# Kernel optimization log

Hardware: AMD Instinct MI355X
Metric: run time of the kernel (lower is better)

Reference implementation:

```python
import jax, jax.numpy as jnp
import numpy as np

B, L, C, V, SU, SI, D = 256, 3, 8, 20, 32, 32, 64
NE, NR = 200000, 32


def _xavier(key, shape):
    fan_in, fan_out = shape[-2], shape[-1]
    a = (6.0 / (fan_in + fan_out)) ** 0.5
    return jax.random.uniform(key, shape, jnp.float32, -a, a)


def setup_inputs() -> dict:
    key = jax.random.key(0)
    ks = jax.random.split(key, 18)

    def triple(k, S):
        k1, k2 = jax.random.split(k)
        ents = jax.random.randint(k1, (B, L, C, 2, S), 0, NE, dtype=jnp.int32)
        rels = jax.random.randint(k2, (B, L, C, 1, S), 0, NR, dtype=jnp.int32)
        # rows: [head, relation, tail]
        return jnp.concatenate([ents[:, :, :, :1], rels, ents[:, :, :, 1:]], axis=3)

    entity_emb = _xavier(ks[0], (NE + 1, D)).at[NE].set(0.0)  # padding row zeroed
    relation_emb = _xavier(ks[1], (NR, D))
    return {
        "user_course_videos": jax.random.randint(ks[2], (B, C, V), 0, NE, dtype=jnp.int32),
        "items": jax.random.randint(ks[3], (B,), 0, NE, dtype=jnp.int32),
        "neg_items": jax.random.randint(ks[4], (B,), 0, NE, dtype=jnp.int32),
        "user_triple_set": triple(ks[5], SU),
        "item_triple_set": triple(ks[6], SI),
        "neg_item_triple_set": triple(ks[7], SI),
        "user_course_list": jax.random.randint(ks[8], (B, C), 0, NE, dtype=jnp.int32),
        "item_course_list": jax.random.randint(ks[9], (B, C), 0, NE, dtype=jnp.int32),
        "neg_item_course_list": jax.random.randint(ks[10], (B, C), 0, NE, dtype=jnp.int32),
        "entity_emb": entity_emb,
        "relation_emb": relation_emb,
        "W": _xavier(ks[11], (2 * D, D)),
        "W_ht": _xavier(ks[12], (2 * D, D)),
        "W_course": _xavier(ks[13], (D, D)),
        "W_video": _xavier(ks[14], (D, D)),
    }


def _normalize(x):
    n = jnp.linalg.norm(x, axis=-1, keepdims=True)
    return x / jnp.maximum(n, 1e-12)


def _layer_emb(E, R, W, W_ht, ts, cce, vce):
    # ts: [B, L, C, 3, S]; cce/vce: [B, D]
    h = E[ts[:, :, :, 0, :]]  # [B,L,C,S,D]
    r = R[ts[:, :, :, 1, :]]
    t = E[ts[:, :, :, 2, :]]
    hr_W = jnp.concatenate([h, r], axis=-1) @ W  # [B,L,C,S,D]
    p = jax.nn.softmax(jax.nn.sigmoid(jnp.einsum('blcsd,bd->blcs', hr_W, cce)), axis=-1)[..., None]
    o = p * t
    if vce is not None:
        ht_W = jnp.concatenate([h, t], axis=-1) @ W_ht
        p2 = jax.nn.sigmoid(jnp.einsum('blcsd,bd->blcs', ht_W, vce))[..., None]
        o = p2 * o
    return o.sum(axis=-2)  # [B,L,C,D]


def _run_user(E, R, W, W_ht, W_course, W_video, ucv, uts, ucl):
    vc = E[ucv].sum(axis=-2)                                     # [B,C,D]
    cce = (E[ucl] + jax.nn.sigmoid(vc @ W_course)).mean(axis=-2)  # [B,D]
    vce = jax.nn.sigmoid(vc.mean(axis=-2) @ W_video)              # [B,D]
    u = _layer_emb(E, R, W, W_ht, uts, cce, vce)                  # [B,L,C,D]
    u = _normalize(jnp.transpose(u, (0, 2, 1, 3)))                # [B,C,L,D]; dropout is identity (eval)
    return u.sum(axis=2).mean(axis=1)                             # [B,D]


def _run_item(E, R, W, W_ht, items, its, icl):
    ie = E[items]                                                 # [B,D]
    cce = ie + ie * E[icl[:, 1:]].mean(axis=-2)                   # [B,D]
    c = _layer_emb(E, R, W, W_ht, its, cce, None)                 # [B,L,C,D]
    c = _normalize(jnp.transpose(c, (0, 2, 1, 3))).sum(axis=2)    # [B,C,D]
    cw = jax.nn.sigmoid(jnp.einsum('bcd,bd->bc', c[:, 1:], c[:, 0]))[..., None]  # [B,C-1,1]
    p_cw = jax.nn.softmax(cw, axis=1)
    mean_cf = (p_cw * c[:, 1:]).sum(axis=1)                       # [B,D]
    alpha = jax.nn.sigmoid((ie * mean_cf).sum(axis=-1, keepdims=True))
    return alpha / (1.0 + alpha) * mean_cf + c[:, 0] + ie


def reference(user_course_videos, items, neg_items, user_triple_set, item_triple_set,
              neg_item_triple_set, user_course_list, item_course_list, neg_item_course_list,
              entity_emb, relation_emb, W, W_ht, W_course, W_video):
    u = _run_user(entity_emb, relation_emb, W, W_ht, W_course, W_video,
                  user_course_videos, user_triple_set, user_course_list)
    c = _run_item(entity_emb, relation_emb, W, W_ht, items, item_triple_set, item_course_list)
    n_c = _run_item(entity_emb, relation_emb, W, W_ht, neg_items, neg_item_triple_set, neg_item_course_list)
    scores = (u * c).sum(axis=1)
    neg_scores = (u * n_c).sum(axis=1)
    return scores, neg_scores
```

## Files before the change

kernel.cpp:

```cpp
#include <hip/hip_runtime.h>
#include <math.h>

#define BB 256
#define LL 3
#define CC 8
#define VV 20
#define SS 32
#define DD 64
#define NG (BB * LL * CC)

typedef float v4f __attribute__((ext_vector_type(4)));

__device__ __forceinline__ float sigmoidf_(float x) { return 1.0f / (1.0f + __expf(-x)); }
__device__ __forceinline__ float dot4v_(v4f a, v4f b) {
    return a[0] * b[0] + a[1] * b[1] + a[2] * b[2] + a[3] * b[3];
}
__device__ __forceinline__ void gload4(v4f& dst, const float* p) {
    asm volatile("global_load_dwordx4 %0, %1, off" : "=v"(dst) : "v"(p));
}

__global__ __launch_bounds__(256) void prologue(
    const float* __restrict__ E, const int* __restrict__ ucv, const int* __restrict__ ucl,
    const int* __restrict__ items, const int* __restrict__ icl, const int* __restrict__ negs,
    const int* __restrict__ ncl, const float* __restrict__ W, const float* __restrict__ W_ht,
    const float* __restrict__ Wc, const float* __restrict__ Wv, float* __restrict__ wcce_u,
    float* __restrict__ whv_u, float* __restrict__ wcce_i, float* __restrict__ wcce_n,
    float* __restrict__ ie_i, float* __restrict__ ie_n) {
    int b = blockIdx.x, tid = threadIdx.x;
    int d = tid & 63, q = tid >> 6;
    __shared__ float vcs[CC][DD];
    __shared__ float part[4][DD];
    __shared__ float part2[4][DD];
    __shared__ float cce_u_s[DD], vce_u_s[DD], cce_i_s[DD], cce_n_s[DD], vmean_s[DD];
    __shared__ float ie_s[2][DD];

    float p1 = 0.f;
    for (int cc = 0; cc < 2; ++cc) {
        int c = q + cc * 4;
        const int* iv = ucv + (b * CC + c) * VV;
        float a = 0.f;
#pragma unroll
        for (int v = 0; v < VV; ++v) a += E[(long)iv[v] * DD + d];
        vcs[c][d] = a;
        p1 += E[(long)ucl[b * CC + c] * DD + d];
    }
    part[q][d] = p1;
    __syncthreads();
    {
        float sacc = 0.f;
        for (int cc = 0; cc < 2; ++cc) {
            int c = q + cc * 4;
            float m = 0.f;
#pragma unroll 8
            for (int k = 0; k < DD; ++k) m += vcs[c][k] * Wc[k * DD + d];
            sacc += sigmoidf_(m);
        }
        part2[q][d] = sacc;
    }
    __syncthreads();
    if (q == 0) {
        float s = 0.f;
#pragma unroll
        for (int i = 0; i < 4; ++i) s += part[i][d] + part2[i][d];
        cce_u_s[d] = s * (1.f / CC);
        float vm = 0.f;
#pragma unroll
        for (int c = 0; c < CC; ++c) vm += vcs[c][d];
        vmean_s[d] = vm * (1.f / CC);
    }
    __syncthreads();
    {
        float m = 0.f;
        for (int k = q * 16; k < q * 16 + 16; ++k) m += vmean_s[k] * Wv[k * DD + d];
        part[q][d] = m;
    }
    {
        const int* cl = (q < 2) ? icl : ncl;
        int c0 = (q & 1) ? 5 : 1, c1 = (q & 1) ? 8 : 5;
        float m = 0.f;
        for (int c = c0; c < c1; ++c) m += E[(long)cl[b * CC + c] * DD + d];
        part2[q][d] = m;
        if (q == 1) ie_s[0][d] = E[(long)items[b] * DD + d];
        if (q == 3) ie_s[1][d] = E[(long)negs[b] * DD + d];
    }
    __syncthreads();
    if (q == 0) {
        vce_u_s[d] = sigmoidf_(part[0][d] + part[1][d] + part[2][d] + part[3][d]);
        float ie = ie_s[0][d];
        cce_i_s[d] = ie * (1.f + (part2[0][d] + part2[1][d]) * (1.f / 7.f));
        ie_i[b * DD + d] = ie;
    } else if (q == 1) {
        float ie = ie_s[1][d];
        cce_n_s[d] = ie * (1.f + (part2[2][d] + part2[3][d]) * (1.f / 7.f));
        ie_n[b * DD + d] = ie;
    }
    __syncthreads();
    {
        int k = tid & 127, sel = tid >> 7;
        const float* wr = (sel ? W_ht : W) + k * DD;
        const float* wr2 = W + k * DD;
        const float* v1 = sel ? vce_u_s : cce_u_s;
        const float* v2 = sel ? cce_n_s : cce_i_s;
        float a = 0.f, c2 = 0.f;
#pragma unroll 8
        for (int kk = 0; kk < DD; ++kk) {
            a += wr[kk] * v1[kk];
            c2 += wr2[kk] * v2[kk];
        }
        if (sel == 0) {
            wcce_u[b * 128 + k] = a;
            wcce_i[b * 128 + k] = c2;
        } else {
            whv_u[b * 128 + k] = a;
            wcce_n[b * 128 + k] = c2;
        }
    }
}

__global__ __launch_bounds__(256, 3) void layer_all(
    const float* __restrict__ E, const float* __restrict__ R, const int* __restrict__ uts,
    const int* __restrict__ its, const int* __restrict__ nts, const float* __restrict__ wcce_u,
    const float* __restrict__ whv_u, const float* __restrict__ wcce_i,
    const float* __restrict__ wcce_n, float* __restrict__ o_all) {
    int tid = threadIdx.x;
    int w = tid >> 6, lane = tid & 63;
    int f = lane & 15, grp = lane >> 4;
    int gg = blockIdx.x * 4 + w;
    int seg = gg / NG;
    int g = gg - seg * NG;
    int b = g / (LL * CC);
    const int* ts = (seg == 0) ? uts : (seg == 1) ? its : nts;
    const float* wcp = (seg == 0) ? wcce_u : (seg == 1) ? wcce_i : wcce_n;
    const bool has_p2 = (seg == 0);
    const int* tg = ts + (long)g * 3 * SS;

    int idx_a = tg[lane];
    int idx_b = tg[64 + (lane & 31)];

    int hix[8], rix[8], tix[8];
#pragma unroll
    for (int p = 0; p < 8; ++p) {
        int row = p * 4 + grp;
        hix[p] = __shfl(idx_a, row, 64);
        rix[p] = __shfl(idx_a, 32 + row, 64);
        tix[p] = __shfl(idx_b, row, 64);
    }

    v4f wc_h, wc_r, wh_h, wh_t;
    gload4(wc_h, wcp + b * 128 + f * 4);
    gload4(wc_r, wcp + b * 128 + 64 + f * 4);
    if (has_p2) {
        gload4(wh_h, whv_u + b * 128 + f * 4);
        gload4(wh_t, whv_u + b * 128 + 64 + f * 4);
    }
    v4f hv[8], rv[8], t4[8];
#pragma unroll
    for (int p = 0; p < 8; ++p) gload4(hv[p], E + (long)hix[p] * DD + f * 4);
#pragma unroll
    for (int p = 0; p < 8; ++p) gload4(rv[p], R + (long)rix[p] * DD + f * 4);
#pragma unroll
    for (int p = 0; p < 8; ++p) gload4(t4[p], E + (long)tix[p] * DD + f * 4);

    asm volatile("s_waitcnt vmcnt(8)");
    __builtin_amdgcn_sched_barrier(0);

    float s1[8];
#pragma unroll
    for (int p = 0; p < 8; ++p) {
        float a1 = dot4v_(hv[p], wc_h) + dot4v_(rv[p], wc_r);
#pragma unroll
        for (int m = 1; m < 16; m <<= 1) a1 += __shfl_xor(a1, m, 64);
        s1[p] = a1;
    }
    float mx = -1e30f;
#pragma unroll
    for (int p = 0; p < 8; ++p) {
        s1[p] = sigmoidf_(s1[p]);
        mx = fmaxf(mx, s1[p]);
    }
    mx = fmaxf(mx, __shfl_xor(mx, 16, 64));
    mx = fmaxf(mx, __shfl_xor(mx, 32, 64));
    float se = 0.f;
#pragma unroll
    for (int p = 0; p < 8; ++p) {
        s1[p] = __expf(s1[p] - mx);
        se += s1[p];
    }
    se += __shfl_xor(se, 16, 64);
    se += __shfl_xor(se, 32, 64);
    float inv = 1.f / se;

    __builtin_amdgcn_sched_barrier(0);
    asm volatile("s_waitcnt vmcnt(0)");
    __builtin_amdgcn_sched_barrier(0);

    float s2[8];
    if (has_p2) {
#pragma unroll
        for (int p = 0; p < 8; ++p) {
            float a2 = dot4v_(hv[p], wh_h) + dot4v_(t4[p], wh_t);
#pragma unroll
            for (int m = 1; m < 16; m <<= 1) a2 += __shfl_xor(a2, m, 64);
            s2[p] = a2;
        }
    }
    float4 oacc = make_float4(0.f, 0.f, 0.f, 0.f);
#pragma unroll
    for (int p = 0; p < 8; ++p) {
        float wgt = s1[p] * inv;
        if (has_p2) wgt *= sigmoidf_(s2[p]);
        oacc.x += wgt * t4[p][0];
        oacc.y += wgt * t4[p][1];
        oacc.z += wgt * t4[p][2];
        oacc.w += wgt * t4[p][3];
    }
#pragma unroll
    for (int m = 16; m <= 32; m <<= 1) {
        oacc.x += __shfl_xor(oacc.x, m, 64);
        oacc.y += __shfl_xor(oacc.y, m, 64);
        oacc.z += __shfl_xor(oacc.z, m, 64);
        oacc.w += __shfl_xor(oacc.w, m, 64);
    }
    float qq = oacc.x * oacc.x + oacc.y * oacc.y + oacc.z * oacc.z + oacc.w * oacc.w;
#pragma unroll
    for (int m = 1; m < 16; m <<= 1) qq += __shfl_xor(qq, m, 64);
    float innorm = 1.f / fmaxf(sqrtf(qq), 1e-12f);
    if (grp == 0) {
        oacc.x *= innorm;
        oacc.y *= innorm;
        oacc.z *= innorm;
        oacc.w *= innorm;
        *(float4*)(o_all + (long)gg * DD + f * 4) = oacc;
    }
}

__global__ __launch_bounds__(192) void postlude(const float* __restrict__ o_all,
                                                const float* __restrict__ ie_i,
                                                const float* __restrict__ ie_n,
                                                float* __restrict__ out) {
    int b = blockIdx.x, tid = threadIdx.x;
    int w = tid / 64, d = tid & 63;
    __shared__ float u_s[DD], ci_s[DD], cn_s[DD];
    if (w == 0) {
        const float* o_u = o_all + (long)b * LL * CC * DD;
        float acc = 0.f;
#pragma unroll
        for (int lc = 0; lc < LL * CC; ++lc) acc += o_u[lc * DD + d];
        u_s[d] = acc * (1.f / CC);
    } else {
        const float* o_c = o_all + ((long)w * NG + (long)b * LL * CC) * DD;
        const float* ie_buf = (w == 1) ? ie_i : ie_n;
        float cs[CC];
#pragma unroll
        for (int c = 0; c < CC; ++c) {
            float a = 0.f;
#pragma unroll
            for (int l = 0; l < LL; ++l) a += o_c[(l * CC + c) * DD + d];
            cs[c] = a;
        }
        float p[CC - 1];
        float mx = -1e30f;
        for (int c = 0; c < CC - 1; ++c) {
            float dd2 = cs[0] * cs[c + 1];
#pragma unroll
            for (int m = 32; m > 0; m >>= 1) dd2 += __shfl_xor(dd2, m, 64);
            p[c] = sigmoidf_(dd2);
            mx = fmaxf(mx, p[c]);
        }
        float se = 0.f;
        for (int c = 0; c < CC - 1; ++c) {
            p[c] = __expf(p[c] - mx);
            se += p[c];
        }
        float mcf = 0.f;
        for (int c = 0; c < CC - 1; ++c) mcf += (p[c] / se) * cs[c + 1];
        float ie = ie_buf[b * DD + d];
        float ad = ie * mcf;
#pragma unroll
        for (int m = 32; m > 0; m >>= 1) ad += __shfl_xor(ad, m, 64);
        float alpha = sigmoidf_(ad);
        float res = alpha / (1.f + alpha) * mcf + cs[0] + ie;
        if (w == 1)
            ci_s[d] = res;
        else
            cn_s[d] = res;
    }
    __syncthreads();
    if (w == 0) {
        float uv = u_s[d];
        float s1 = uv * ci_s[d];
        float s2 = uv * cn_s[d];
#pragma unroll
        for (int m = 32; m > 0; m >>= 1) {
            s1 += __shfl_xor(s1, m, 64);
            s2 += __shfl_xor(s2, m, 64);
        }
        if (d == 0) {
            out[b] = s1;
            out[BB + b] = s2;
        }
    }
}

extern "C" void kernel_launch(void* const* d_in, const int* in_sizes, int n_in,
                              void* d_out, int out_size, void* d_ws, size_t ws_size,
                              hipStream_t stream) {
    const int* ucv = (const int*)d_in[0];
    const int* items = (const int*)d_in[1];
    const int* negs = (const int*)d_in[2];
    const int* uts = (const int*)d_in[3];
    const int* its = (const int*)d_in[4];
    const int* nts = (const int*)d_in[5];
    const int* ucl = (const int*)d_in[6];
    const int* icl = (const int*)d_in[7];
    const int* ncl = (const int*)d_in[8];
    const float* E = (const float*)d_in[9];
    const float* R = (const float*)d_in[10];
    const float* W = (const float*)d_in[11];
    const float* W_ht = (const float*)d_in[12];
    const float* Wc = (const float*)d_in[13];
    const float* Wv = (const float*)d_in[14];

    float* ws = (float*)d_ws;
    float* wcce_u = ws;
    float* whv_u = wcce_u + BB * 128;
    float* wcce_i = whv_u + BB * 128;
    float* wcce_n = wcce_i + BB * 128;
    float* ie_i = wcce_n + BB * 128;
    float* ie_n = ie_i + BB * DD;
    float* o_all = ie_n + BB * DD;

    prologue<<<BB, 256, 0, stream>>>(E, ucv, ucl, items, icl, negs, ncl, W, W_ht, Wc, Wv,
                                     wcce_u, whv_u, wcce_i, wcce_n, ie_i, ie_n);
    layer_all<<<(3 * NG) / 4, 256, 0, stream>>>(E, R, uts, its, nts, wcce_u, whv_u, wcce_i,
                                                wcce_n, o_all);
    postlude<<<BB, 192, 0, stream>>>(o_all, ie_i, ie_n, (float*)d_out);
}
```

Baseline: 65.15 us.

## Gather triple embeddings directly into LDS via global_load_lds with one-wave blocks

Replaces the register-destined gathers of head, relation and tail embeddings with global_load_lds transfers into a 24KB shared staging buffer, then reads the rows back from LDS. Each block now holds a single wave and handles one group, so the launch has four times as many blocks. The goal is to cut VGPR pressure from the 24 in-flight vector loads and raise occupancy for this latency-bound gather. In exchange it adds an LDS round trip and a large per-block LDS footprint that caps waves per CU. It also relies on the vmcnt-based waits covering the LDS-bound DMA loads.

```diff
diff --git a/kernel.cpp b/kernel.cpp
--- a/kernel.cpp
+++ b/kernel.cpp
@@ -15,8 +15,10 @@
 __device__ __forceinline__ float dot4v_(v4f a, v4f b) {
     return a[0] * b[0] + a[1] * b[1] + a[2] * b[2] + a[3] * b[3];
 }
-__device__ __forceinline__ void gload4(v4f& dst, const float* p) {
-    asm volatile("global_load_dwordx4 %0, %1, off" : "=v"(dst) : "v"(p));
+__device__ __forceinline__ void gl_lds16(const float* gsrc, float* lptr) {
+    __builtin_amdgcn_global_load_lds(
+        (const __attribute__((address_space(1))) void*)(uintptr_t)gsrc,
+        (__attribute__((address_space(3))) void*)(uint32_t)(uintptr_t)lptr, 16, 0, 0);
 }
 
 __global__ __launch_bounds__(256) void prologue(
@@ -117,15 +119,14 @@
     }
 }
 
-__global__ __launch_bounds__(256, 3) void layer_all(
+__global__ __launch_bounds__(64) void layer_all(
     const float* __restrict__ E, const float* __restrict__ R, const int* __restrict__ uts,
     const int* __restrict__ its, const int* __restrict__ nts, const float* __restrict__ wcce_u,
     const float* __restrict__ whv_u, const float* __restrict__ wcce_i,
     const float* __restrict__ wcce_n, float* __restrict__ o_all) {
-    int tid = threadIdx.x;
-    int w = tid >> 6, lane = tid & 63;
+    int lane = threadIdx.x;
     int f = lane & 15, grp = lane >> 4;
-    int gg = blockIdx.x * 4 + w;
+    int gg = blockIdx.x;
     int seg = gg / NG;
     int g = gg - seg * NG;
     int b = g / (LL * CC);
@@ -134,40 +135,46 @@
     const bool has_p2 = (seg == 0);
     const int* tg = ts + (long)g * 3 * SS;
 
+    __shared__ float stage[96 * DD];
+
     int idx_a = tg[lane];
     int idx_b = tg[64 + (lane & 31)];
 
-    int hix[8], rix[8], tix[8];
+    v4f wch = *(const v4f*)(wcp + b * 128 + f * 4);
+    v4f wcr = *(const v4f*)(wcp + b * 128 + 64 + f * 4);
+    v4f whh = {0.f, 0.f, 0.f, 0.f}, wht = {0.f, 0.f, 0.f, 0.f};
+    if (has_p2) {
+        whh = *(const v4f*)(whv_u + b * 128 + f * 4);
+        wht = *(const v4f*)(whv_u + b * 128 + 64 + f * 4);
+    }
+    __builtin_amdgcn_sched_barrier(0);
+
+#pragma unroll
+    for (int q = 0; q < 8; ++q) {
+        int hi = __shfl(idx_a, q * 4 + grp, 64);
+        gl_lds16(E + (long)hi * DD + f * 4, stage + (q * 4) * DD);
+    }
+#pragma unroll
+    for (int q = 0; q < 8; ++q) {
+        int ri = __shfl(idx_a, 32 + q * 4 + grp, 64);
+        gl_lds16(R + (long)ri * DD + f * 4, stage + (32 + q * 4) * DD);
+    }
+#pragma unroll
+    for (int q = 0; q < 8; ++q) {
+        int ti = __shfl(idx_b, q * 4 + grp, 64);
+        gl_lds16(E + (long)ti * DD + f * 4, stage + (64 + q * 4) * DD);
+    }
+
+    asm volatile("s_waitcnt vmcnt(8)" ::: "memory");
+    __builtin_amdgcn_sched_barrier(0);
+
+    v4f hv[8];
+    float s1[8];
 #pragma unroll
     for (int p = 0; p < 8; ++p) {
-        int row = p * 4 + grp;
-        hix[p] = __shfl(idx_a, row, 64);
-        rix[p] = __shfl(idx_a, 32 + row, 64);
-        tix[p] = __shfl(idx_b, row, 64);
-    }
-
-    v4f wc_h, wc_r, wh_h, wh_t;
-    gload4(wc_h, wcp + b * 128 + f * 4);
-    gload4(wc_r, wcp + b * 128 + 64 + f * 4);
-    if (has_p2) {
-        gload4(wh_h, whv_u + b * 128 + f * 4);
-        gload4(wh_t, whv_u + b * 128 + 64 + f * 4);
-    }
-    v4f hv[8], rv[8], t4[8];
-#pragma unroll
-    for (int p = 0; p < 8; ++p) gload4(hv[p], E + (long)hix[p] * DD + f * 4);
-#pragma unroll
-    for (int p = 0; p < 8; ++p) gload4(rv[p], R + (long)rix[p] * DD + f * 4);
-#pragma unroll
-    for (int p = 0; p < 8; ++p) gload4(t4[p], E + (long)tix[p] * DD + f * 4);
-
-    asm volatile("s_waitcnt vmcnt(8)");
-    __builtin_amdgcn_sched_barrier(0);
-
-    float s1[8];
-#pragma unroll
-    for (int p = 0; p < 8; ++p) {
-        float a1 = dot4v_(hv[p], wc_h) + dot4v_(rv[p], wc_r);
+        hv[p] = *(const v4f*)(stage + (p * 4 + grp) * DD + f * 4);
+        v4f rv = *(const v4f*)(stage + (32 + p * 4 + grp) * DD + f * 4);
+        float a1 = dot4v_(hv[p], wch) + dot4v_(rv, wcr);
 #pragma unroll
         for (int m = 1; m < 16; m <<= 1) a1 += __shfl_xor(a1, m, 64);
         s1[p] = a1;
@@ -191,28 +198,24 @@
     float inv = 1.f / se;
 
     __builtin_amdgcn_sched_barrier(0);
-    asm volatile("s_waitcnt vmcnt(0)");
+    asm volatile("s_waitcnt vmcnt(0)" ::: "memory");
     __builtin_amdgcn_sched_barrier(0);
 
-    float s2[8];
-    if (has_p2) {
-#pragma unroll
-        for (int p = 0; p < 8; ++p) {
-            float a2 = dot4v_(hv[p], wh_h) + dot4v_(t4[p], wh_t);
+    float4 oacc = make_float4(0.f, 0.f, 0.f, 0.f);
+#pragma unroll
+    for (int p = 0; p < 8; ++p) {
+        v4f t4 = *(const v4f*)(stage + (64 + p * 4 + grp) * DD + f * 4);
+        float wgt = s1[p] * inv;
+        if (has_p2) {
+            float a2 = dot4v_(hv[p], whh) + dot4v_(t4, wht);
 #pragma unroll
             for (int m = 1; m < 16; m <<= 1) a2 += __shfl_xor(a2, m, 64);
-            s2[p] = a2;
-        }
-    }
-    float4 oacc = make_float4(0.f, 0.f, 0.f, 0.f);
-#pragma unroll
-    for (int p = 0; p < 8; ++p) {
-        float wgt = s1[p] * inv;
-        if (has_p2) wgt *= sigmoidf_(s2[p]);
-        oacc.x += wgt * t4[p][0];
-        oacc.y += wgt * t4[p][1];
-        oacc.z += wgt * t4[p][2];
-        oacc.w += wgt * t4[p][3];
+            wgt *= sigmoidf_(a2);
+        }
+        oacc.x += wgt * t4[0];
+        oacc.y += wgt * t4[1];
+        oacc.z += wgt * t4[2];
+        oacc.w += wgt * t4[3];
     }
 #pragma unroll
     for (int m = 16; m <= 32; m <<= 1) {
@@ -332,7 +335,7 @@
 
     prologue<<<BB, 256, 0, stream>>>(E, ucv, ucl, items, icl, negs, ncl, W, W_ht, Wc, Wv,
                                      wcce_u, whv_u, wcce_i, wcce_n, ie_i, ie_n);
-    layer_all<<<(3 * NG) / 4, 256, 0, stream>>>(E, R, uts, its, nts, wcce_u, whv_u, wcce_i,
-                                                wcce_n, o_all);
+    layer_all<<<3 * NG, 64, 0, stream>>>(E, R, uts, its, nts, wcce_u, whv_u, wcce_i,
+                                         wcce_n, o_all);
     postlude<<<BB, 192, 0, stream>>>(o_all, ie_i, ie_n, (float*)d_out);
 }
```

New measurement: 82.61 us. 1.27x slower.

## Make layer kernel persistent grid-stride and drop inline-asm loads and waitcnts

Applied to the files above, without the earlier changes.

The layer kernel goes from one wave per group with 4-wave blocks to a persistent grid-stride loop over 4096 waves in 2-wave blocks with a higher occupancy hint. The hand-written global_load asm and explicit vmcnt waits are replaced by plain vector loads, so the compiler now schedules loads and the s2 computation. The aim is to cut block launch overhead and let the compiler overlap loads across loop iterations. In exchange it gives up the manual split that started the softmax while the tail loads were still in flight, and each wave now handles several groups in sequence.

```diff
diff --git a/kernel.cpp b/kernel.cpp
--- a/kernel.cpp
+++ b/kernel.cpp
@@ -8,15 +8,13 @@
 #define SS 32
 #define DD 64
 #define NG (BB * LL * CC)
+#define NWAVES 4096
 
 typedef float v4f __attribute__((ext_vector_type(4)));
 
 __device__ __forceinline__ float sigmoidf_(float x) { return 1.0f / (1.0f + __expf(-x)); }
 __device__ __forceinline__ float dot4v_(v4f a, v4f b) {
     return a[0] * b[0] + a[1] * b[1] + a[2] * b[2] + a[3] * b[3];
-}
-__device__ __forceinline__ void gload4(v4f& dst, const float* p) {
-    asm volatile("global_load_dwordx4 %0, %1, off" : "=v"(dst) : "v"(p));
 }
 
 __global__ __launch_bounds__(256) void prologue(
@@ -117,120 +115,113 @@
     }
 }
 
-__global__ __launch_bounds__(256, 3) void layer_all(
+__global__ __launch_bounds__(128, 8) void layer_all(
     const float* __restrict__ E, const float* __restrict__ R, const int* __restrict__ uts,
     const int* __restrict__ its, const int* __restrict__ nts, const float* __restrict__ wcce_u,
     const float* __restrict__ whv_u, const float* __restrict__ wcce_i,
     const float* __restrict__ wcce_n, float* __restrict__ o_all) {
     int tid = threadIdx.x;
-    int w = tid >> 6, lane = tid & 63;
+    int lane = tid & 63;
     int f = lane & 15, grp = lane >> 4;
-    int gg = blockIdx.x * 4 + w;
-    int seg = gg / NG;
-    int g = gg - seg * NG;
-    int b = g / (LL * CC);
-    const int* ts = (seg == 0) ? uts : (seg == 1) ? its : nts;
-    const float* wcp = (seg == 0) ? wcce_u : (seg == 1) ? wcce_i : wcce_n;
-    const bool has_p2 = (seg == 0);
-    const int* tg = ts + (long)g * 3 * SS;
-
-    int idx_a = tg[lane];
-    int idx_b = tg[64 + (lane & 31)];
-
-    int hix[8], rix[8], tix[8];
-#pragma unroll
-    for (int p = 0; p < 8; ++p) {
-        int row = p * 4 + grp;
-        hix[p] = __shfl(idx_a, row, 64);
-        rix[p] = __shfl(idx_a, 32 + row, 64);
-        tix[p] = __shfl(idx_b, row, 64);
-    }
-
-    v4f wc_h, wc_r, wh_h, wh_t;
-    gload4(wc_h, wcp + b * 128 + f * 4);
-    gload4(wc_r, wcp + b * 128 + 64 + f * 4);
-    if (has_p2) {
-        gload4(wh_h, whv_u + b * 128 + f * 4);
-        gload4(wh_t, whv_u + b * 128 + 64 + f * 4);
-    }
-    v4f hv[8], rv[8], t4[8];
-#pragma unroll
-    for (int p = 0; p < 8; ++p) gload4(hv[p], E + (long)hix[p] * DD + f * 4);
-#pragma unroll
-    for (int p = 0; p < 8; ++p) gload4(rv[p], R + (long)rix[p] * DD + f * 4);
-#pragma unroll
-    for (int p = 0; p < 8; ++p) gload4(t4[p], E + (long)tix[p] * DD + f * 4);
-
-    asm volatile("s_waitcnt vmcnt(8)");
-    __builtin_amdgcn_sched_barrier(0);
-
-    float s1[8];
-#pragma unroll
-    for (int p = 0; p < 8; ++p) {
-        float a1 = dot4v_(hv[p], wc_h) + dot4v_(rv[p], wc_r);
-#pragma unroll
-        for (int m = 1; m < 16; m <<= 1) a1 += __shfl_xor(a1, m, 64);
-        s1[p] = a1;
-    }
-    float mx = -1e30f;
-#pragma unroll
-    for (int p = 0; p < 8; ++p) {
-        s1[p] = sigmoidf_(s1[p]);
-        mx = fmaxf(mx, s1[p]);
-    }
-    mx = fmaxf(mx, __shfl_xor(mx, 16, 64));
-    mx = fmaxf(mx, __shfl_xor(mx, 32, 64));
-    float se = 0.f;
-#pragma unroll
-    for (int p = 0; p < 8; ++p) {
-        s1[p] = __expf(s1[p] - mx);
-        se += s1[p];
-    }
-    se += __shfl_xor(se, 16, 64);
-    se += __shfl_xor(se, 32, 64);
-    float inv = 1.f / se;
-
-    __builtin_amdgcn_sched_barrier(0);
-    asm volatile("s_waitcnt vmcnt(0)");
-    __builtin_amdgcn_sched_barrier(0);
-
-    float s2[8];
-    if (has_p2) {
-#pragma unroll
-        for (int p = 0; p < 8; ++p) {
-            float a2 = dot4v_(hv[p], wh_h) + dot4v_(t4[p], wh_t);
-#pragma unroll
-            for (int m = 1; m < 16; m <<= 1) a2 += __shfl_xor(a2, m, 64);
-            s2[p] = a2;
-        }
-    }
-    float4 oacc = make_float4(0.f, 0.f, 0.f, 0.f);
-#pragma unroll
-    for (int p = 0; p < 8; ++p) {
-        float wgt = s1[p] * inv;
-        if (has_p2) wgt *= sigmoidf_(s2[p]);
-        oacc.x += wgt * t4[p][0];
-        oacc.y += wgt * t4[p][1];
-        oacc.z += wgt * t4[p][2];
-        oacc.w += wgt * t4[p][3];
-    }
-#pragma unroll
-    for (int m = 16; m <= 32; m <<= 1) {
-        oacc.x += __shfl_xor(oacc.x, m, 64);
-        oacc.y += __shfl_xor(oacc.y, m, 64);
-        oacc.z += __shfl_xor(oacc.z, m, 64);
-        oacc.w += __shfl_xor(oacc.w, m, 64);
-    }
-    float qq = oacc.x * oacc.x + oacc.y * oacc.y + oacc.z * oacc.z + oacc.w * oacc.w;
-#pragma unroll
-    for (int m = 1; m < 16; m <<= 1) qq += __shfl_xor(qq, m, 64);
-    float innorm = 1.f / fmaxf(sqrtf(qq), 1e-12f);
-    if (grp == 0) {
-        oacc.x *= innorm;
-        oacc.y *= innorm;
-        oacc.z *= innorm;
-        oacc.w *= innorm;
-        *(float4*)(o_all + (long)gg * DD + f * 4) = oacc;
+    int wave0 = blockIdx.x * 2 + (tid >> 6);
+
+    for (int gg = wave0; gg < 3 * NG; gg += NWAVES) {
+        int seg = gg / NG;
+        int g = gg - seg * NG;
+        int b = g / (LL * CC);
+        const int* ts = (seg == 0) ? uts : (seg == 1) ? its : nts;
+        const float* wcp = (seg == 0) ? wcce_u : (seg == 1) ? wcce_i : wcce_n;
+        const bool has_p2 = (seg == 0);
+        const int* tg = ts + (long)g * 3 * SS;
+
+        int idx_a = tg[lane];
+        int idx_b = tg[64 + (lane & 31)];
+        int hix[8], rix[8], tix[8];
+#pragma unroll
+        for (int p = 0; p < 8; ++p) {
+            int row = p * 4 + grp;
+            hix[p] = __shfl(idx_a, row, 64);
+            rix[p] = __shfl(idx_a, 32 + row, 64);
+            tix[p] = __shfl(idx_b, row, 64);
+        }
+        const v4f* wc4 = (const v4f*)(wcp + b * 128);
+        v4f wc_h = wc4[f], wc_r = wc4[f + 16];
+        v4f wh_h = {0.f, 0.f, 0.f, 0.f}, wh_t = wh_h;
+        if (has_p2) {
+            const v4f* wh4 = (const v4f*)(whv_u + b * 128);
+            wh_h = wh4[f];
+            wh_t = wh4[f + 16];
+        }
+        v4f hv[8], rv[8], t4[8];
+#pragma unroll
+        for (int p = 0; p < 8; ++p) hv[p] = *(const v4f*)(E + (long)hix[p] * DD + f * 4);
+#pragma unroll
+        for (int p = 0; p < 8; ++p) rv[p] = *(const v4f*)(R + (long)rix[p] * DD + f * 4);
+#pragma unroll
+        for (int p = 0; p < 8; ++p) t4[p] = *(const v4f*)(E + (long)tix[p] * DD + f * 4);
+
+        float s1[8], s2[8];
+#pragma unroll
+        for (int p = 0; p < 8; ++p) {
+            float a1 = dot4v_(hv[p], wc_h) + dot4v_(rv[p], wc_r);
+#pragma unroll
+            for (int m = 1; m < 16; m <<= 1) a1 += __shfl_xor(a1, m, 64);
+            s1[p] = a1;
+        }
+        if (has_p2) {
+#pragma unroll
+            for (int p = 0; p < 8; ++p) {
+                float a2 = dot4v_(hv[p], wh_h) + dot4v_(t4[p], wh_t);
+#pragma unroll
+                for (int m = 1; m < 16; m <<= 1) a2 += __shfl_xor(a2, m, 64);
+                s2[p] = a2;
+            }
+        }
+        float mx = -1e30f;
+#pragma unroll
+        for (int p = 0; p < 8; ++p) {
+            s1[p] = sigmoidf_(s1[p]);
+            mx = fmaxf(mx, s1[p]);
+        }
+        mx = fmaxf(mx, __shfl_xor(mx, 16, 64));
+        mx = fmaxf(mx, __shfl_xor(mx, 32, 64));
+        float se = 0.f;
+#pragma unroll
+        for (int p = 0; p < 8; ++p) {
+            s1[p] = __expf(s1[p] - mx);
+            se += s1[p];
+        }
+        se += __shfl_xor(se, 16, 64);
+        se += __shfl_xor(se, 32, 64);
+        float inv = 1.f / se;
+        float4 oacc = make_float4(0.f, 0.f, 0.f, 0.f);
+#pragma unroll
+        for (int p = 0; p < 8; ++p) {
+            float wgt = s1[p] * inv;
+            if (has_p2) wgt *= sigmoidf_(s2[p]);
+            oacc.x += wgt * t4[p][0];
+            oacc.y += wgt * t4[p][1];
+            oacc.z += wgt * t4[p][2];
+            oacc.w += wgt * t4[p][3];
+        }
+#pragma unroll
+        for (int m = 16; m <= 32; m <<= 1) {
+            oacc.x += __shfl_xor(oacc.x, m, 64);
+            oacc.y += __shfl_xor(oacc.y, m, 64);
+            oacc.z += __shfl_xor(oacc.z, m, 64);
+            oacc.w += __shfl_xor(oacc.w, m, 64);
+        }
+        float qq = oacc.x * oacc.x + oacc.y * oacc.y + oacc.z * oacc.z + oacc.w * oacc.w;
+#pragma unroll
+        for (int m = 1; m < 16; m <<= 1) qq += __shfl_xor(qq, m, 64);
+        float innorm = 1.f / fmaxf(sqrtf(qq), 1e-12f);
+        if (grp == 0) {
+            oacc.x *= innorm;
+            oacc.y *= innorm;
+            oacc.z *= innorm;
+            oacc.w *= innorm;
+            *(float4*)(o_all + (long)gg * DD + f * 4) = oacc;
+        }
     }
 }
 
@@ -332,7 +323,7 @@
 
     prologue<<<BB, 256, 0, stream>>>(E, ucv, ucl, items, icl, negs, ncl, W, W_ht, Wc, Wv,
                                      wcce_u, whv_u, wcce_i, wcce_n, ie_i, ie_n);
-    layer_all<<<(3 * NG) / 4, 256, 0, stream>>>(E, R, uts, its, nts, wcce_u, whv_u, wcce_i,
-                                                wcce_n, o_all);
+    layer_all<<<NWAVES / 2, 128, 0, stream>>>(E, R, uts, its, nts, wcce_u, whv_u, wcce_i,
+                                              wcce_n, o_all);
     postlude<<<BB, 192, 0, stream>>>(o_all, ie_i, ie_n, (float*)d_out);
 }
```

Result: slower. 187.2 us (+187.3%).
